# Kernel optimization log

Hardware: AMD Instinct MI355X
Metric: run time of the kernel (lower is better)

## Reference

```python
import jax, jax.numpy as jnp
import numpy as np

N = 60000   # nodes per siamese side
E = 960000  # edges per side (avg degree 16)
B = 32      # graphs per batch
F = 38      # input node features
H = 128     # h_ch == out_ch
EPS = 1e-5


def graph_conv(x, edge_index, W_rel, W_root, b):
    # PyG GraphConv (aggr='add'): lin_rel(sum_j x_j) + lin_root(x_i) + bias
    src, dst = edge_index[0], edge_index[1]
    agg = jax.ops.segment_sum(x[src], dst, num_segments=x.shape[0])
    return agg @ W_rel + x @ W_root + b


def batch_norm(x, gamma, beta):
    # training-mode BN over the node dimension (biased variance)
    mu = x.mean(axis=0)
    var = x.var(axis=0)
    return (x - mu) * jax.lax.rsqrt(var + EPS) * gamma + beta


def embed(x, edge_index, batch,
          W1r, W1s, b1, g1, be1,
          W2r, W2s, b2, g2, be2,
          W3r, W3s, b3, g3, be3,
          Wg1, bg1, Wg2, bg2):
    h1 = jax.nn.relu(batch_norm(graph_conv(x, edge_index, W1r, W1s, b1), g1, be1))
    h2 = jax.nn.relu(batch_norm(graph_conv(h1, edge_index, W2r, W2s, b2), g2, be2))
    ho = jax.nn.relu(batch_norm(graph_conv(h2, edge_index, W3r, W3s, b3), g3, be3))
    # GlobalAttentionSelect, pool_ref='last': gate from last conv output
    gate = jax.nn.relu(jax.nn.relu(ho @ Wg1 + bg1) @ Wg2 + bg2)  # [N,1]
    gmax = jax.ops.segment_max(gate, batch, num_segments=B)       # [B,1]
    eg = jnp.exp(gate - gmax[batch])
    denom = jax.ops.segment_sum(eg, batch, num_segments=B)
    attn = eg / denom[batch]                                      # per-graph softmax
    return jax.ops.segment_sum(attn * ho, batch, num_segments=B)  # [B,H]


def setup_inputs() -> dict:
    key = jax.random.key(0)
    ks = jax.random.split(key, 40)
    s = 0.05
    inp = {
        "x1": jax.random.normal(ks[0], (N, F), dtype=jnp.float32),
        "x2": jax.random.normal(ks[1], (N, F), dtype=jnp.float32),
        "edge_index1": jax.random.randint(ks[2], (2, E), 0, N),
        "edge_index2": jax.random.randint(ks[3], (2, E), 0, N),
        "batch1": jnp.sort(jax.random.randint(ks[4], (N,), 0, B)),
        "batch2": jnp.sort(jax.random.randint(ks[5], (N,), 0, B)),
        # conv1: F->H
        "W1r": jax.random.normal(ks[6], (F, H), dtype=jnp.float32) * s,
        "W1s": jax.random.normal(ks[7], (F, H), dtype=jnp.float32) * s,
        "b1": jnp.zeros((H,), jnp.float32),
        "g1": jnp.ones((H,), jnp.float32), "be1": jnp.zeros((H,), jnp.float32),
        # conv2: H->H
        "W2r": jax.random.normal(ks[8], (H, H), dtype=jnp.float32) * s,
        "W2s": jax.random.normal(ks[9], (H, H), dtype=jnp.float32) * s,
        "b2": jnp.zeros((H,), jnp.float32),
        "g2": jnp.ones((H,), jnp.float32), "be2": jnp.zeros((H,), jnp.float32),
        # conv_out: H->H
        "W3r": jax.random.normal(ks[10], (H, H), dtype=jnp.float32) * s,
        "W3s": jax.random.normal(ks[11], (H, H), dtype=jnp.float32) * s,
        "b3": jnp.zeros((H,), jnp.float32),
        "g3": jnp.ones((H,), jnp.float32), "be3": jnp.zeros((H,), jnp.float32),
        # gate MLP: H->32->1 (final ReLU)
        "Wg1": jax.random.normal(ks[12], (H, 32), dtype=jnp.float32) * s,
        "bg1": jnp.zeros((32,), jnp.float32),
        "Wg2": jax.random.normal(ks[13], (32, 1), dtype=jnp.float32) * s,
        "bg2": jnp.zeros((1,), jnp.float32),
        # final MLP on |e1-e2|: H->64->1
        "Wf1": jax.random.normal(ks[14], (H, 64), dtype=jnp.float32) * s,
        "bf1": jnp.zeros((64,), jnp.float32),
        "Wf2": jax.random.normal(ks[15], (64, 1), dtype=jnp.float32) * s,
        "bf2": jnp.zeros((1,), jnp.float32),
    }
    return inp


def reference(x1, x2, edge_index1, edge_index2, batch1, batch2,
              W1r, W1s, b1, g1, be1,
              W2r, W2s, b2, g2, be2,
              W3r, W3s, b3, g3, be3,
              Wg1, bg1, Wg2, bg2,
              Wf1, bf1, Wf2, bf2):
    e1 = embed(x1, edge_index1, batch1, W1r, W1s, b1, g1, be1,
               W2r, W2s, b2, g2, be2, W3r, W3s, b3, g3, be3,
               Wg1, bg1, Wg2, bg2)
    e2 = embed(x2, edge_index2, batch2, W1r, W1s, b1, g1, be1,
               W2r, W2s, b2, g2, be2, W3r, W3s, b3, g3, be3,
               Wg1, bg1, Wg2, bg2)
    d = jnp.abs(e1 - e2)                       # final_out_join='abs'
    out = jax.nn.relu(d @ Wf1 + bf1) @ Wf2 + bf2  # [B,1]
    return out
```

## Files before the change

### kernel.cpp

```cpp
#include <hip/hip_runtime.h>
#include <cstdint>
#include <cstddef>

#define NN 60000
#define NE 960000
#define NB 32
#define FIN 38
#define HH 128

typedef short bf16x8 __attribute__((ext_vector_type(8)));
typedef float f32x4 __attribute__((ext_vector_type(4)));

__device__ __forceinline__ unsigned short f2bf(float x) {
  unsigned u = __builtin_bit_cast(unsigned, x);
  u = u + 0x7fffu + ((u >> 16) & 1u);
  return (unsigned short)(u >> 16);
}
__device__ __forceinline__ float bf2f(unsigned short h) {
  unsigned u = ((unsigned)h) << 16;
  return __builtin_bit_cast(float, u);
}

__global__ __launch_bounds__(256) void k_hist(const int* __restrict__ ei0,
                                              const int* __restrict__ ei1,
                                              int* __restrict__ counts) {
  int s = blockIdx.y;
  const int* ei = s ? ei1 : ei0;
  int i = blockIdx.x * 256 + threadIdx.x;
  if (i < NE) atomicAdd(&counts[s * NN + ei[NE + i]], 1);
}

__global__ __launch_bounds__(1024) void k_scan(const int* __restrict__ counts_,
                                               int* __restrict__ rowptr_,
                                               int* __restrict__ cursor_) {
  int s = blockIdx.x;
  const int* counts = counts_ + (size_t)s * NN;
  int* rowptr = rowptr_ + (size_t)s * (NN + 1);
  int* cursor = cursor_ + (size_t)s * NN;
  __shared__ int sm[1024];
  const int C = 59;
  int t = threadIdx.x;
  int base = t * C;
  int lsum = 0;
  for (int j = 0; j < C; ++j) {
    int idx = base + j;
    if (idx < NN) lsum += counts[idx];
  }
  sm[t] = lsum;
  __syncthreads();
  for (int off = 1; off < 1024; off <<= 1) {
    int v = (t >= off) ? sm[t - off] : 0;
    __syncthreads();
    sm[t] += v;
    __syncthreads();
  }
  int run = sm[t] - lsum;
  for (int j = 0; j < C; ++j) {
    int idx = base + j;
    if (idx < NN) {
      rowptr[idx] = run;
      cursor[idx] = run;
      run += counts[idx];
    }
  }
  if (t == 1023) rowptr[NN] = sm[1023];
}

__global__ __launch_bounds__(256) void k_scatter(const int* __restrict__ ei0,
                                                 const int* __restrict__ ei1,
                                                 int* __restrict__ cursor,
                                                 int* __restrict__ col) {
  int s = blockIdx.y;
  const int* ei = s ? ei1 : ei0;
  int i = blockIdx.x * 256 + threadIdx.x;
  if (i < NE) {
    int dst = ei[NE + i];
    int src = ei[i];
    int pos = atomicAdd(&cursor[s * NN + dst], 1);
    col[(size_t)s * NE + pos] = src;
  }
}

template <int W>
__global__ __launch_bounds__(256) void k_agg(const float* __restrict__ h0,
                                             const float* __restrict__ h1,
                                             const int* __restrict__ rowptr_,
                                             const int* __restrict__ col_,
                                             float* __restrict__ agg_) {
  int s = blockIdx.y;
  const float* h = s ? h1 : h0;
  const int* rowptr = rowptr_ + (size_t)s * (NN + 1);
  const int* col = col_ + (size_t)s * NE;
  float* agg = agg_ + (size_t)s * NN * W;
  int wave = threadIdx.x >> 6;
  int lane = threadIdx.x & 63;
  int node = blockIdx.x * 4 + wave;
  if (node >= NN) return;
  int s0 = rowptr[node], s1 = rowptr[node + 1];
  if (W == 128) {
    float2 acc = make_float2(0.f, 0.f);
    const float* hp = h + (lane << 1);
    int j = s0;
    for (; j + 3 < s1; j += 4) {
      int a0 = col[j], a1 = col[j + 1], a2 = col[j + 2], a3 = col[j + 3];
      float2 v0 = *reinterpret_cast<const float2*>(hp + (size_t)a0 * 128);
      float2 v1 = *reinterpret_cast<const float2*>(hp + (size_t)a1 * 128);
      float2 v2 = *reinterpret_cast<const float2*>(hp + (size_t)a2 * 128);
      float2 v3 = *reinterpret_cast<const float2*>(hp + (size_t)a3 * 128);
      acc.x += (v0.x + v1.x) + (v2.x + v3.x);
      acc.y += (v0.y + v1.y) + (v2.y + v3.y);
    }
    for (; j < s1; ++j) {
      int a0 = col[j];
      float2 v0 = *reinterpret_cast<const float2*>(hp + (size_t)a0 * 128);
      acc.x += v0.x;
      acc.y += v0.y;
    }
    *reinterpret_cast<float2*>(agg + (size_t)node * 128 + (lane << 1)) = acc;
  } else {
    float2 acc = make_float2(0.f, 0.f);
    if (lane < 19) {
      const float* hp = h + (lane << 1);
      int j = s0;
      for (; j + 1 < s1; j += 2) {
        int a0 = col[j], a1 = col[j + 1];
        float2 v0 = *reinterpret_cast<const float2*>(hp + (size_t)a0 * W);
        float2 v1 = *reinterpret_cast<const float2*>(hp + (size_t)a1 * W);
        acc.x += v0.x + v1.x;
        acc.y += v0.y + v1.y;
      }
      if (j < s1) {
        float2 v = *reinterpret_cast<const float2*>(hp + (size_t)col[j] * W);
        acc.x += v.x;
        acc.y += v.y;
      }
      *reinterpret_cast<float2*>(agg + (size_t)node * W + (lane << 1)) = acc;
    }
  }
}

template <bool VEC>
__global__ __launch_bounds__(256) void k_gemm_mfma(
    const float* __restrict__ A_, int lda, const float* __restrict__ X0,
    const float* __restrict__ X1, int ldx, const float* __restrict__ Wr,
    const float* __restrict__ Ws, const float* __restrict__ bias, int K,
    float* __restrict__ Z_, float* __restrict__ stats_) {
  int side = blockIdx.y;
  const float* A = A_ + (size_t)side * NN * lda;
  const float* X = side ? X1 : X0;
  float* Z = Z_ + (size_t)side * NN * HH;
  float* stats = stats_ + (size_t)side * 256;

  __shared__ __align__(16) unsigned char sAh[64 * 64];
  __shared__ __align__(16) unsigned char sAl[64 * 64];
  __shared__ __align__(16) unsigned char sXh[64 * 64];
  __shared__ __align__(16) unsigned char sXl[64 * 64];
  __shared__ __align__(16) unsigned char sBh[2][128 * 64];
  __shared__ __align__(16) unsigned char sBl[2][128 * 64];

  int t = threadIdx.x;
  int l = t & 63;
  int wid = t >> 6;
  int wr = wid >> 1, wc = wid & 1;
  int row0 = blockIdx.x * 64;

  f32x4 acc[2][4];
#pragma unroll
  for (int rt = 0; rt < 2; ++rt)
#pragma unroll
    for (int ct = 0; ct < 4; ++ct) acc[rt][ct] = (f32x4)(0.f);

  int nK = (K + 31) >> 5;
  for (int ks = 0; ks < nK; ++ks) {
    {
      int r = t >> 2;
      int kc = (t & 3) << 3;
      int grow = row0 + r;
      float av[8], xv[8];
      if (VEC) {
        float4 a0 = make_float4(0, 0, 0, 0), a1 = a0, x0 = a0, x1 = a0;
        if (grow < NN) {
          const float* pa = A + (size_t)grow * lda + (ks << 5) + kc;
          const float* px = X + (size_t)grow * ldx + (ks << 5) + kc;
          a0 = *reinterpret_cast<const float4*>(pa);
          a1 = *reinterpret_cast<const float4*>(pa + 4);
          x0 = *reinterpret_cast<const float4*>(px);
          x1 = *reinterpret_cast<const float4*>(px + 4);
        }
        av[0] = a0.x; av[1] = a0.y; av[2] = a0.z; av[3] = a0.w;
        av[4] = a1.x; av[5] = a1.y; av[6] = a1.z; av[7] = a1.w;
        xv[0] = x0.x; xv[1] = x0.y; xv[2] = x0.z; xv[3] = x0.w;
        xv[4] = x1.x; xv[5] = x1.y; xv[6] = x1.z; xv[7] = x1.w;
      } else {
#pragma unroll
        for (int e = 0; e < 8; ++e) {
          int gk = (ks << 5) + kc + e;
          bool ok = (grow < NN) && (gk < K);
          av[e] = ok ? A[(size_t)grow * lda + gk] : 0.f;
          xv[e] = ok ? X[(size_t)grow * ldx + gk] : 0.f;
        }
      }
      bf16x8 ah, al, xh, xl;
#pragma unroll
      for (int e = 0; e < 8; ++e) {
        unsigned short h = f2bf(av[e]);
        ah[e] = (short)h;
        al[e] = (short)f2bf(av[e] - bf2f(h));
        h = f2bf(xv[e]);
        xh[e] = (short)h;
        xl[e] = (short)f2bf(xv[e] - bf2f(h));
      }
      int off = ((r << 6) + (kc << 1)) ^ ((r & 7) << 4);
      *reinterpret_cast<bf16x8*>(sAh + off) = ah;
      *reinterpret_cast<bf16x8*>(sAl + off) = al;
      *reinterpret_cast<bf16x8*>(sXh + off) = xh;
      *reinterpret_cast<bf16x8*>(sXl + off) = xl;
    }
    {
      int kq = t >> 5;
      int c0 = (t & 31) << 2;
      float wf[2][4][4];
#pragma unroll
      for (int kk = 0; kk < 4; ++kk) {
        int gk = (ks << 5) + (kq << 2) + kk;
        float4 vr = make_float4(0, 0, 0, 0), vs = vr;
        if (gk < K) {
          vr = *reinterpret_cast<const float4*>(Wr + (size_t)gk * HH + c0);
          vs = *reinterpret_cast<const float4*>(Ws + (size_t)gk * HH + c0);
        }
        wf[0][kk][0] = vr.x; wf[0][kk][1] = vr.y; wf[0][kk][2] = vr.z; wf[0][kk][3] = vr.w;
        wf[1][kk][0] = vs.x; wf[1][kk][1] = vs.y; wf[1][kk][2] = vs.z; wf[1][kk][3] = vs.w;
      }
#pragma unroll
      for (int m = 0; m < 2; ++m) {
#pragma unroll
        for (int j = 0; j < 4; ++j) {
          int c = c0 + j;
          unsigned h0 = f2bf(wf[m][0][j]), h1 = f2bf(wf[m][1][j]);
          unsigned h2 = f2bf(wf[m][2][j]), h3 = f2bf(wf[m][3][j]);
          unsigned l0 = f2bf(wf[m][0][j] - bf2f((unsigned short)h0));
          unsigned l1 = f2bf(wf[m][1][j] - bf2f((unsigned short)h1));
          unsigned l2 = f2bf(wf[m][2][j] - bf2f((unsigned short)h2));
          unsigned l3 = f2bf(wf[m][3][j] - bf2f((unsigned short)h3));
          uint2 hv = make_uint2(h0 | (h1 << 16), h2 | (h3 << 16));
          uint2 lv = make_uint2(l0 | (l1 << 16), l2 | (l3 << 16));
          int off = ((c << 6) + (kq << 3)) ^ ((c & 7) << 4);
          *reinterpret_cast<uint2*>(sBh[m] + off) = hv;
          *reinterpret_cast<uint2*>(sBl[m] + off) = lv;
        }
      }
    }
    __syncthreads();
    bf16x8 fah[2], fal[2], fxh[2], fxl[2];
    int ko = (l >> 4) << 4;
#pragma unroll
    for (int rt = 0; rt < 2; ++rt) {
      int rr = (wr << 5) + (rt << 4) + (l & 15);
      int off = ((rr << 6) + ko) ^ ((rr & 7) << 4);
      fah[rt] = *reinterpret_cast<const bf16x8*>(sAh + off);
      fal[rt] = *reinterpret_cast<const bf16x8*>(sAl + off);
      fxh[rt] = *reinterpret_cast<const bf16x8*>(sXh + off);
      fxl[rt] = *reinterpret_cast<const bf16x8*>(sXl + off);
    }
#pragma unroll
    for (int ct = 0; ct < 4; ++ct) {
      int cc = (wc << 6) + (ct << 4) + (l & 15);
      int off = ((cc << 6) + ko) ^ ((cc & 7) << 4);
      bf16x8 brh = *reinterpret_cast<const bf16x8*>(sBh[0] + off);
      bf16x8 brl = *reinterpret_cast<const bf16x8*>(sBl[0] + off);
      bf16x8 bsh = *reinterpret_cast<const bf16x8*>(sBh[1] + off);
      bf16x8 bsl = *reinterpret_cast<const bf16x8*>(sBl[1] + off);
#pragma unroll
      for (int rt = 0; rt < 2; ++rt) {
        f32x4 c = acc[rt][ct];
        c = __builtin_amdgcn_mfma_f32_16x16x32_bf16(fah[rt], brh, c, 0, 0, 0);
        c = __builtin_amdgcn_mfma_f32_16x16x32_bf16(fah[rt], brl, c, 0, 0, 0);
        c = __builtin_amdgcn_mfma_f32_16x16x32_bf16(fal[rt], brh, c, 0, 0, 0);
        c = __builtin_amdgcn_mfma_f32_16x16x32_bf16(fxh[rt], bsh, c, 0, 0, 0);
        c = __builtin_amdgcn_mfma_f32_16x16x32_bf16(fxh[rt], bsl, c, 0, 0, 0);
        c = __builtin_amdgcn_mfma_f32_16x16x32_bf16(fxl[rt], bsh, c, 0, 0, 0);
        acc[rt][ct] = c;
      }
    }
    __syncthreads();
  }

  float ps[4] = {0, 0, 0, 0}, pq[4] = {0, 0, 0, 0};
#pragma unroll
  for (int ct = 0; ct < 4; ++ct) {
    int col = (wc << 6) + (ct << 4) + (l & 15);
    float b = bias[col];
#pragma unroll
    for (int rt = 0; rt < 2; ++rt) {
      int rbase = row0 + (wr << 5) + (rt << 4) + ((l >> 4) << 2);
      f32x4 v = acc[rt][ct];
#pragma unroll
      for (int rg = 0; rg < 4; ++rg) {
        int row = rbase + rg;
        if (row < NN) {
          float z = v[rg] + b;
          Z[(size_t)row * HH + col] = z;
          ps[ct] += z;
          pq[ct] += z * z;
        }
      }
    }
  }
#pragma unroll
  for (int ct = 0; ct < 4; ++ct) {
    ps[ct] += __shfl_xor(ps[ct], 16, 64);
    ps[ct] += __shfl_xor(ps[ct], 32, 64);
    pq[ct] += __shfl_xor(pq[ct], 16, 64);
    pq[ct] += __shfl_xor(pq[ct], 32, 64);
  }
  if (l < 16) {
#pragma unroll
    for (int ct = 0; ct < 4; ++ct) {
      int col = (wc << 6) + (ct << 4) + l;
      atomicAdd(&stats[col], ps[ct]);
      atomicAdd(&stats[HH + col], pq[ct]);
    }
  }
}

__global__ void k_bnfin(const float* __restrict__ stats_, const float* __restrict__ g,
                        const float* __restrict__ be, float* __restrict__ ss_) {
  int s = blockIdx.x;
  const float* stats = stats_ + (size_t)s * 256;
  float* ss = ss_ + (size_t)s * 256;
  int c = threadIdx.x;
  if (c < HH) {
    float mu = stats[c] * (1.0f / NN);
    float var = stats[HH + c] * (1.0f / NN) - mu * mu;
    float inv = 1.0f / sqrtf(var + 1e-5f);
    float sc = g[c] * inv;
    ss[c] = sc;
    ss[HH + c] = be[c] - mu * sc;
  }
}

__global__ __launch_bounds__(256) void k_bnrelu(float* __restrict__ ZH_,
                                                const float* __restrict__ ss_) {
  int s = blockIdx.y;
  float* ZH = ZH_ + (size_t)s * NN * HH;
  const float* ss = ss_ + (size_t)s * 256;
  size_t i = (size_t)blockIdx.x * 256 + threadIdx.x;
  float4 z = *reinterpret_cast<float4*>(ZH + i * 4);
  int c = (int)((i * 4) & 127);
  float4 sc = *reinterpret_cast<const float4*>(ss + c);
  float4 sh = *reinterpret_cast<const float4*>(ss + HH + c);
  z.x = fmaxf(z.x * sc.x + sh.x, 0.f);
  z.y = fmaxf(z.y * sc.y + sh.y, 0.f);
  z.z = fmaxf(z.z * sc.z + sh.z, 0.f);
  z.w = fmaxf(z.w * sc.w + sh.w, 0.f);
  *reinterpret_cast<float4*>(ZH + i * 4) = z;
}

__global__ __launch_bounds__(256) void k_gate(const float* __restrict__ Ho_,
                                              const float* __restrict__ Wg1,
                                              const float* __restrict__ bg1,
                                              const float* __restrict__ Wg2,
                                              const float* __restrict__ bg2,
                                              float* __restrict__ gate_) {
  int s = blockIdx.y;
  const float* Ho = Ho_ + (size_t)s * NN * HH;
  float* gate = gate_ + (size_t)s * NN;
  __shared__ float sW[128 * 32];
  int t = threadIdx.x;
  for (int i = t; i < 128 * 32 / 4; i += 256)
    *reinterpret_cast<float4*>(&sW[i * 4]) =
        *reinterpret_cast<const float4*>(Wg1 + i * 4);
  __syncthreads();
  int lane = t & 63, wv = t >> 6;
  int half = lane >> 5, l = lane & 31;
  float w2 = Wg2[l];
  float b2 = bg2[0];
  float b1v = bg1[l];
  for (int it = 0; it < 16; ++it) {
    int node = blockIdx.x * 128 + it * 8 + wv * 2 + half;
    if (node < NN) {
      const float* hr = Ho + (size_t)node * 128;
      float acc = b1v;
      for (int k = 0; k < 128; k += 4) {
        float4 hv = *reinterpret_cast<const float4*>(hr + k);
        acc += hv.x * sW[(k) * 32 + l];
        acc += hv.y * sW[(k + 1) * 32 + l];
        acc += hv.z * sW[(k + 2) * 32 + l];
        acc += hv.w * sW[(k + 3) * 32 + l];
      }
      float v = fmaxf(acc, 0.f) * w2;
#pragma unroll
      for (int off = 16; off > 0; off >>= 1) v += __shfl_down(v, off, 32);
      if (l == 0) gate[node] = fmaxf(v + b2, 0.f);
    }
  }
}

__global__ void k_bounds(const int* __restrict__ batch0,
                         const int* __restrict__ batch1,
                         int* __restrict__ starts, int* __restrict__ ends) {
  int s = blockIdx.x;
  const int* batch = s ? batch1 : batch0;
  int g = threadIdx.x;
  if (g >= NB) return;
  int lo = 0, hi = NN;
  while (lo < hi) { int mid = (lo + hi) >> 1; if (batch[mid] < g) lo = mid + 1; else hi = mid; }
  starts[s * NB + g] = lo;
  lo = 0; hi = NN;
  while (lo < hi) { int mid = (lo + hi) >> 1; if (batch[mid] < g + 1) lo = mid + 1; else hi = mid; }
  ends[s * NB + g] = lo;
}

__global__ __launch_bounds__(256) void k_gstat(const float* __restrict__ gate_,
                                               const int* __restrict__ starts,
                                               const int* __restrict__ ends,
                                               float* __restrict__ gm,
                                               float* __restrict__ dn) {
  int sd = blockIdx.y;
  int b = blockIdx.x;
  const float* gate = gate_ + (size_t)sd * NN;
  __shared__ float red[256];
  int t = threadIdx.x;
  int s = starts[sd * NB + b], en = ends[sd * NB + b];
  float m = -3.402823e38f;
  for (int i = s + t; i < en; i += 256) m = fmaxf(m, gate[i]);
  red[t] = m;
  __syncthreads();
  for (int off = 128; off > 0; off >>= 1) {
    if (t < off) red[t] = fmaxf(red[t], red[t + off]);
    __syncthreads();
  }
  float gmax = red[0];
  __syncthreads();
  float ds = 0;
  for (int i = s + t; i < en; i += 256) ds += expf(gate[i] - gmax);
  red[t] = ds;
  __syncthreads();
  for (int off = 128; off > 0; off >>= 1) {
    if (t < off) red[t] += red[t + off];
    __syncthreads();
  }
  if (t == 0) {
    gm[sd * NB + b] = gmax;
    dn[sd * NB + b] = red[0];
  }
}

#define SPL 8
__global__ __launch_bounds__(256) void k_poolsum(const float* __restrict__ Ho_,
                                                 const float* __restrict__ gate_,
                                                 const int* __restrict__ starts,
                                                 const int* __restrict__ ends,
                                                 const float* __restrict__ gm,
                                                 const float* __restrict__ dn,
                                                 float* __restrict__ e) {
  int sd = blockIdx.y;
  int b = blockIdx.x;
  int z = blockIdx.z;
  const float* Ho = Ho_ + (size_t)sd * NN * HH;
  const float* gate = gate_ + (size_t)sd * NN;
  __shared__ float red[256];
  int t = threadIdx.x;
  int s = starts[sd * NB + b], en = ends[sd * NB + b];
  int len = en - s;
  if (len <= 0) return;
  int chunk = (len + SPL - 1) / SPL;
  int i0 = s + z * chunk;
  int i1 = min(en, i0 + chunk);
  if (i0 >= i1) return;
  float gmax = gm[sd * NB + b];
  float invdn = 1.0f / dn[sd * NB + b];
  int c = t & 127, half = t >> 7;
  float acc = 0;
  for (int i = i0 + half; i < i1; i += 2)
    acc += expf(gate[i] - gmax) * Ho[(size_t)i * 128 + c];
  red[t] = acc;
  __syncthreads();
  if (t < 128)
    atomicAdd(&e[(size_t)sd * NB * HH + (size_t)b * HH + t],
              (red[t] + red[t + 128]) * invdn);
}

__global__ void k_final(const float* __restrict__ e, const float* __restrict__ Wf1,
                        const float* __restrict__ bf1, const float* __restrict__ Wf2,
                        const float* __restrict__ bf2, float* __restrict__ out) {
  int b = blockIdx.x, j = threadIdx.x;
  float acc = bf1[j];
  const float* e1 = e + (size_t)b * 128;
  const float* e2 = e + (size_t)NB * 128 + (size_t)b * 128;
  for (int k = 0; k < 128; ++k) {
    float d = fabsf(e1[k] - e2[k]);
    acc += d * Wf1[k * 64 + j];
  }
  float v = fmaxf(acc, 0.f) * Wf2[j];
#pragma unroll
  for (int off = 32; off > 0; off >>= 1) v += __shfl_down(v, off, 64);
  if (j == 0) out[b] = v + bf2[0];
}

extern "C" void kernel_launch(void* const* d_in, const int* in_sizes, int n_in,
                              void* d_out, int out_size, void* d_ws, size_t ws_size,
                              hipStream_t stream) {
  const float* x0 = (const float*)d_in[0];
  const float* x1 = (const float*)d_in[1];
  const int* ei0 = (const int*)d_in[2];
  const int* ei1 = (const int*)d_in[3];
  const int* batch0 = (const int*)d_in[4];
  const int* batch1 = (const int*)d_in[5];
  const float* W1r = (const float*)d_in[6];
  const float* W1s = (const float*)d_in[7];
  const float* b1 = (const float*)d_in[8];
  const float* g1 = (const float*)d_in[9];
  const float* be1 = (const float*)d_in[10];
  const float* W2r = (const float*)d_in[11];
  const float* W2s = (const float*)d_in[12];
  const float* b2 = (const float*)d_in[13];
  const float* g2 = (const float*)d_in[14];
  const float* be2 = (const float*)d_in[15];
  const float* W3r = (const float*)d_in[16];
  const float* W3s = (const float*)d_in[17];
  const float* b3 = (const float*)d_in[18];
  const float* g3 = (const float*)d_in[19];
  const float* be3 = (const float*)d_in[20];
  const float* Wg1 = (const float*)d_in[21];
  const float* bg1 = (const float*)d_in[22];
  const float* Wg2 = (const float*)d_in[23];
  const float* bg2 = (const float*)d_in[24];
  const float* Wf1 = (const float*)d_in[25];
  const float* bf1 = (const float*)d_in[26];
  const float* Wf2 = (const float*)d_in[27];
  const float* bf2 = (const float*)d_in[28];

  char* p = (char*)d_ws;
  auto alloc = [&](size_t bytes) {
    void* r = (void*)p;
    p += (bytes + 255) & ~(size_t)255;
    return r;
  };
  int* counts = (int*)alloc((size_t)2 * NN * 4);
  int* rowptr = (int*)alloc((size_t)2 * (NN + 1) * 4);
  int* cursor = (int*)alloc((size_t)2 * NN * 4);
  int* col = (int*)alloc((size_t)2 * NE * 4);
  int* starts = (int*)alloc(2 * NB * 4);
  int* ends = (int*)alloc(2 * NB * 4);
  float* stats = (float*)alloc(2 * 256 * 4);
  float* ss = (float*)alloc(2 * 256 * 4);
  float* gate = (float*)alloc((size_t)2 * NN * 4);
  float* gm = (float*)alloc(2 * NB * 4);
  float* dn = (float*)alloc(2 * NB * 4);
  float* ebuf = (float*)alloc((size_t)2 * NB * HH * 4);
  float* bufA = (float*)alloc((size_t)2 * NN * HH * 4);
  float* bufB = (float*)alloc((size_t)2 * NN * HH * 4);
  float* bufC = (float*)alloc((size_t)2 * NN * HH * 4);

  hipMemsetAsync(counts, 0, (size_t)2 * NN * 4, stream);
  k_hist<<<dim3((NE + 255) / 256, 2), 256, 0, stream>>>(ei0, ei1, counts);
  k_scan<<<2, 1024, 0, stream>>>(counts, rowptr, cursor);
  k_scatter<<<dim3((NE + 255) / 256, 2), 256, 0, stream>>>(ei0, ei1, cursor, col);

  k_agg<38><<<dim3(15000, 2), 256, 0, stream>>>(x0, x1, rowptr, col, bufA);
  hipMemsetAsync(stats, 0, 2 * 256 * 4, stream);
  k_gemm_mfma<false><<<dim3(938, 2), 256, 0, stream>>>(
      bufA, FIN, x0, x1, FIN, W1r, W1s, b1, FIN, bufB, stats);
  k_bnfin<<<2, 128, 0, stream>>>(stats, g1, be1, ss);
  k_bnrelu<<<dim3(7500, 2), 256, 0, stream>>>(bufB, ss);

  k_agg<128><<<dim3(15000, 2), 256, 0, stream>>>(bufB, bufB + (size_t)NN * HH,
                                                 rowptr, col, bufA);
  hipMemsetAsync(stats, 0, 2 * 256 * 4, stream);
  k_gemm_mfma<true><<<dim3(938, 2), 256, 0, stream>>>(
      bufA, HH, bufB, bufB + (size_t)NN * HH, HH, W2r, W2s, b2, HH, bufC, stats);
  k_bnfin<<<2, 128, 0, stream>>>(stats, g2, be2, ss);
  k_bnrelu<<<dim3(7500, 2), 256, 0, stream>>>(bufC, ss);

  k_agg<128><<<dim3(15000, 2), 256, 0, stream>>>(bufC, bufC + (size_t)NN * HH,
                                                 rowptr, col, bufA);
  hipMemsetAsync(stats, 0, 2 * 256 * 4, stream);
  k_gemm_mfma<true><<<dim3(938, 2), 256, 0, stream>>>(
      bufA, HH, bufC, bufC + (size_t)NN * HH, HH, W3r, W3s, b3, HH, bufB, stats);
  k_bnfin<<<2, 128, 0, stream>>>(stats, g3, be3, ss);
  k_bnrelu<<<dim3(7500, 2), 256, 0, stream>>>(bufB, ss);

  k_gate<<<dim3(469, 2), 256, 0, stream>>>(bufB, Wg1, bg1, Wg2, bg2, gate);
  k_bounds<<<2, 32, 0, stream>>>(batch0, batch1, starts, ends);
  hipMemsetAsync(ebuf, 0, (size_t)2 * NB * HH * 4, stream);
  k_gstat<<<dim3(NB, 2), 256, 0, stream>>>(gate, starts, ends, gm, dn);
  k_poolsum<<<dim3(NB, 2, SPL), 256, 0, stream>>>(bufB, gate, starts, ends, gm, dn,
                                                  ebuf);

  k_final<<<NB, 64, 0, stream>>>(ebuf, Wf1, bf1, Wf2, bf2, (float*)d_out);
}
```

Before: 1.389 ms.

## Parallelize CSR prefix scan across blocks and store column indices as 16-bit

Replaces the single-block-per-side serial prefix scan with a three-pass multi-block scan (per-block scan, scan of block sums, add offsets), spreading the work over many CUs instead of two. It also narrows the CSR column array from 32-bit to 16-bit unsigned indices, halving index traffic in the scatter and in every aggregation pass. The 16-bit indices only hold because N=60000 fits in an unsigned short, so the code breaks for larger graphs. The scan adds two extra kernel launches.

```diff
diff --git a/kernel.cpp b/kernel.cpp
--- a/kernel.cpp
+++ b/kernel.cpp
@@ -7,6 +7,7 @@
 #define NB 32
 #define FIN 38
 #define HH 128
+#define SCB 235
 
 typedef short bf16x8 __attribute__((ext_vector_type(8)));
 typedef float f32x4 __attribute__((ext_vector_type(4)));
@@ -30,46 +31,61 @@
   if (i < NE) atomicAdd(&counts[s * NN + ei[NE + i]], 1);
 }
 
-__global__ __launch_bounds__(1024) void k_scan(const int* __restrict__ counts_,
+__global__ __launch_bounds__(256) void k_scan1(const int* __restrict__ counts_,
                                                int* __restrict__ rowptr_,
-                                               int* __restrict__ cursor_) {
-  int s = blockIdx.x;
+                                               int* __restrict__ bsum) {
+  int s = blockIdx.y, b = blockIdx.x, t = threadIdx.x;
+  int idx = b * 256 + t;
   const int* counts = counts_ + (size_t)s * NN;
   int* rowptr = rowptr_ + (size_t)s * (NN + 1);
-  int* cursor = cursor_ + (size_t)s * NN;
-  __shared__ int sm[1024];
-  const int C = 59;
-  int t = threadIdx.x;
-  int base = t * C;
-  int lsum = 0;
-  for (int j = 0; j < C; ++j) {
-    int idx = base + j;
-    if (idx < NN) lsum += counts[idx];
-  }
-  sm[t] = lsum;
+  __shared__ int sm[256];
+  int c = (idx < NN) ? counts[idx] : 0;
+  sm[t] = c;
   __syncthreads();
-  for (int off = 1; off < 1024; off <<= 1) {
+  for (int off = 1; off < 256; off <<= 1) {
     int v = (t >= off) ? sm[t - off] : 0;
     __syncthreads();
     sm[t] += v;
     __syncthreads();
   }
-  int run = sm[t] - lsum;
-  for (int j = 0; j < C; ++j) {
-    int idx = base + j;
-    if (idx < NN) {
-      rowptr[idx] = run;
-      cursor[idx] = run;
-      run += counts[idx];
-    }
-  }
-  if (t == 1023) rowptr[NN] = sm[1023];
+  if (idx < NN) rowptr[idx] = sm[t] - c;
+  if (t == 255) bsum[s * SCB + b] = sm[255];
+}
+
+__global__ __launch_bounds__(256) void k_scan2(const int* __restrict__ bsum,
+                                               int* __restrict__ boff,
+                                               int* __restrict__ rowptr_) {
+  int s = blockIdx.x, t = threadIdx.x;
+  __shared__ int sm[256];
+  int v = (t < SCB) ? bsum[s * SCB + t] : 0;
+  sm[t] = v;
+  __syncthreads();
+  for (int off = 1; off < 256; off <<= 1) {
+    int u = (t >= off) ? sm[t - off] : 0;
+    __syncthreads();
+    sm[t] += u;
+    __syncthreads();
+  }
+  if (t < SCB) boff[s * SCB + t] = sm[t] - v;
+  if (t == 255) rowptr_[(size_t)s * (NN + 1) + NN] = sm[255];
+}
+
+__global__ __launch_bounds__(256) void k_scan3(int* __restrict__ rowptr_,
+                                               int* __restrict__ cursor_,
+                                               const int* __restrict__ boff) {
+  int s = blockIdx.y, b = blockIdx.x, t = threadIdx.x;
+  int idx = b * 256 + t;
+  if (idx < NN) {
+    int v = rowptr_[(size_t)s * (NN + 1) + idx] + boff[s * SCB + b];
+    rowptr_[(size_t)s * (NN + 1) + idx] = v;
+    cursor_[(size_t)s * NN + idx] = v;
+  }
 }
 
 __global__ __launch_bounds__(256) void k_scatter(const int* __restrict__ ei0,
                                                  const int* __restrict__ ei1,
                                                  int* __restrict__ cursor,
-                                                 int* __restrict__ col) {
+                                                 unsigned short* __restrict__ col) {
   int s = blockIdx.y;
   const int* ei = s ? ei1 : ei0;
   int i = blockIdx.x * 256 + threadIdx.x;
@@ -77,7 +93,7 @@
     int dst = ei[NE + i];
     int src = ei[i];
     int pos = atomicAdd(&cursor[s * NN + dst], 1);
-    col[(size_t)s * NE + pos] = src;
+    col[(size_t)s * NE + pos] = (unsigned short)src;
   }
 }
 
@@ -85,12 +101,12 @@
 __global__ __launch_bounds__(256) void k_agg(const float* __restrict__ h0,
                                              const float* __restrict__ h1,
                                              const int* __restrict__ rowptr_,
-                                             const int* __restrict__ col_,
+                                             const unsigned short* __restrict__ col_,
                                              float* __restrict__ agg_) {
   int s = blockIdx.y;
   const float* h = s ? h1 : h0;
   const int* rowptr = rowptr_ + (size_t)s * (NN + 1);
-  const int* col = col_ + (size_t)s * NE;
+  const unsigned short* col = col_ + (size_t)s * NE;
   float* agg = agg_ + (size_t)s * NN * W;
   int wave = threadIdx.x >> 6;
   int lane = threadIdx.x & 63;
@@ -540,7 +556,9 @@
   int* counts = (int*)alloc((size_t)2 * NN * 4);
   int* rowptr = (int*)alloc((size_t)2 * (NN + 1) * 4);
   int* cursor = (int*)alloc((size_t)2 * NN * 4);
-  int* col = (int*)alloc((size_t)2 * NE * 4);
+  unsigned short* col = (unsigned short*)alloc((size_t)2 * NE * 2);
+  int* bsum = (int*)alloc(2 * SCB * 4);
+  int* boff = (int*)alloc(2 * SCB * 4);
   int* starts = (int*)alloc(2 * NB * 4);
   int* ends = (int*)alloc(2 * NB * 4);
   float* stats = (float*)alloc(2 * 256 * 4);
@@ -555,7 +573,9 @@
 
   hipMemsetAsync(counts, 0, (size_t)2 * NN * 4, stream);
   k_hist<<<dim3((NE + 255) / 256, 2), 256, 0, stream>>>(ei0, ei1, counts);
-  k_scan<<<2, 1024, 0, stream>>>(counts, rowptr, cursor);
+  k_scan1<<<dim3(SCB, 2), 256, 0, stream>>>(counts, rowptr, bsum);
+  k_scan2<<<2, 256, 0, stream>>>(bsum, boff, rowptr);
+  k_scan3<<<dim3(SCB, 2), 256, 0, stream>>>(rowptr, cursor, boff);
   k_scatter<<<dim3((NE + 255) / 256, 2), 256, 0, stream>>>(ei0, ei1, cursor, col);
 
   k_agg<38><<<dim3(15000, 2), 256, 0, stream>>>(x0, x1, rowptr, col, bufA);
```

New measurement: 1.261 ms. 9.3% less time.
